# Kernel tuning notes

Measured on AMD Instinct MI355X. Metric: run time of the kernel, lower is better.

Reference implementation:

```python
import jax, jax.numpy as jnp
import numpy as np
from math import sqrt

B, T, C = 2, 2048, 2048
H = 16
NOPE, ROPE, VD, LORA = 128, 64, 128, 512
QK = NOPE + ROPE  # 192
EPS = 1e-6


def _make_freq_cis(T, rope_dim):
    inv = 1.0 / (10000.0 ** (np.arange(0, rope_dim, 2, dtype=np.float32) / rope_dim))
    t = np.arange(T, dtype=np.float32)
    ang = np.outer(t, inv)  # [T, rope_dim/2]
    return jnp.asarray(np.stack([np.cos(ang), np.sin(ang)], -1))  # [T, rope_dim/2, 2]


def setup_inputs() -> dict:
    key = jax.random.key(0)
    ks = jax.random.split(key, 6)
    x = jax.random.normal(ks[0], (B, T, C), jnp.float32)
    freq_cis = _make_freq_cis(T, ROPE)
    causal = jnp.where(jnp.tril(jnp.ones((T, T), bool)), 0.0, -1e9).astype(jnp.float32)
    Wq = jax.random.normal(ks[1], (C, H * QK), jnp.float32) * (1.0 / sqrt(C))
    Wckv = jax.random.normal(ks[2], (C, LORA + ROPE), jnp.float32) * (1.0 / sqrt(C))
    kv_norm_w = jnp.ones((LORA,), jnp.float32)
    Wdkv = jax.random.normal(ks[3], (LORA, H * (NOPE + VD)), jnp.float32) * (1.0 / sqrt(LORA))
    Wproj = jax.random.normal(ks[4], (H * VD, C), jnp.float32) * (1.0 / sqrt(H * VD))
    return {"x": x, "freq_cis": freq_cis, "mask": causal, "window": causal,
            "Wq": Wq, "Wckv": Wckv, "kv_norm_w": kv_norm_w, "Wdkv": Wdkv,
            "Wproj": Wproj, "start_pos": 0}


def apply_rope(x, freq_cis):
    # x: [B, T, h, D]; freq_cis: [T, D/2, 2]
    b, t, h, d = x.shape
    xr = x.reshape(b, t, h, d // 2, 2)
    fc = freq_cis.reshape(1, t, 1, d // 2, 2)
    real = xr[..., 0] * fc[..., 0] - xr[..., 1] * fc[..., 1]
    imag = xr[..., 1] * fc[..., 0] + xr[..., 0] * fc[..., 1]
    return jnp.stack([real, imag], -1).reshape(b, t, h, d)


def rms_norm(x, w, eps=EPS):
    return x * jax.lax.rsqrt(jnp.mean(x * x, -1, keepdims=True) + eps) * w


def reference(x, freq_cis, mask, window, Wq, Wckv, kv_norm_w, Wdkv, Wproj, start_pos):
    del window, start_pos  # Global attention, no KV cache (prefill)
    b, t, _ = x.shape
    q = (x @ Wq).reshape(b, t, H, QK)
    q_nope, q_rope = q[..., :NOPE], q[..., NOPE:]
    q_rope = apply_rope(q_rope, freq_cis)

    ckv = x @ Wckv  # [B, T, LORA+ROPE]
    kv_lat, k_rope = ckv[..., :LORA], ckv[..., LORA:]
    k_rope = apply_rope(k_rope.reshape(b, t, 1, ROPE), freq_cis)  # [B,T,1,ROPE]

    kv = rms_norm(kv_lat, kv_norm_w) @ Wdkv  # [B, T, H*(NOPE+VD)]
    kv = kv.reshape(b, t, H, NOPE + VD)
    k_nope, v = kv[..., :NOPE], kv[..., NOPE:]

    q = jnp.concatenate([q_nope, q_rope], -1)                                   # [B,T,H,QK]
    k = jnp.concatenate([k_nope, jnp.broadcast_to(k_rope, (b, t, H, ROPE))], -1)

    scale = 1.0 / sqrt(QK)
    atten = jnp.einsum('bqhd,bkhd->bhqk', q, k) * scale + mask  # [B,H,T,T]
    atten = jax.nn.softmax(atten, -1)
    out = jnp.einsum('bhqk,bkhd->bqhd', atten, v).reshape(b, t, H * VD)
    return out @ Wproj
```

## Files before the change

### kernel.cpp

```cpp
#include <hip/hip_runtime.h>
#include <hip/hip_bf16.h>
#include <math.h>


typedef short bf16x8 __attribute__((ext_vector_type(8)));
typedef float f32x4 __attribute__((ext_vector_type(4)));

#define MFMA16(a, b, c) __builtin_amdgcn_mfma_f32_16x16x32_bf16(a, b, c, 0, 0, 0)

__device__ __forceinline__ short f2bf(float f) {
  union { float f; unsigned u; } v; v.f = f;
  unsigned r = v.u + 0x7fffu + ((v.u >> 16) & 1u);
  return (short)(r >> 16);
}
__device__ __forceinline__ float bf2f(short s) {
  union { unsigned u; float f; } v;
  v.u = ((unsigned)(unsigned short)s) << 16;
  return v.f;
}
__device__ __forceinline__ void gl16(const void* g, void* l) {
  __builtin_amdgcn_global_load_lds(
      (const __attribute__((address_space(1))) unsigned int*)g,
      (__attribute__((address_space(3))) unsigned int*)l, 16, 0, 0);
}
#define CFENCE() asm volatile("" ::: "memory")
#define HWBAR()  do { CFENCE(); __builtin_amdgcn_s_barrier(); CFENCE(); } while (0)

__global__ __launch_bounds__(256) void cvt_k(const float* __restrict__ in,
                                             short* __restrict__ out, int n) {
  int i = (blockIdx.x * 256 + threadIdx.x) * 8;
  if (i >= n) return;
  float4 a = *(const float4*)(in + i);
  float4 b = *(const float4*)(in + i + 4);
  bf16x8 o;
  o[0] = f2bf(a.x); o[1] = f2bf(a.y); o[2] = f2bf(a.z); o[3] = f2bf(a.w);
  o[4] = f2bf(b.x); o[5] = f2bf(b.y); o[6] = f2bf(b.z); o[7] = f2bf(b.w);
  *(bf16x8*)(out + i) = o;
}

__global__ __launch_bounds__(256) void tcvt_k(const float* __restrict__ W,
                                              short* __restrict__ out,
                                              int K, int N, int Np, int row_off) {
  __shared__ float tile[32][33];
  int k0 = blockIdx.x * 32, n0 = blockIdx.y * 32;
  int tx = threadIdx.x & 31, ty = threadIdx.x >> 5;
#pragma unroll
  for (int j = 0; j < 4; j++) {
    int k = k0 + ty + j * 8, n = n0 + tx;
    tile[ty + j * 8][tx] = (n < N) ? W[(size_t)k * N + n] : 0.f;
  }
  __syncthreads();
#pragma unroll
  for (int j = 0; j < 4; j++) {
    int n = n0 + ty + j * 8;
    out[(size_t)(row_off + n) * K + k0 + tx] = f2bf(tile[tx][ty + j * 8]);
  }
}

template <int MODE, int BM, int BN, int SGL>
__global__ __launch_bounds__(512, 2) void gemm8_k(const short* __restrict__ A,
                                                  const short* __restrict__ Bt,
                                                  void* __restrict__ C1,
                                                  void* __restrict__ C2,
                                                  int M, int N, int K, int nbx) {
  constexpr int FM = BM / 32;
  constexpr int FN = BN / 64;
  constexpr int XCH = (BM * 4) / 512;
  constexpr int YCH = (BN * 4) / 512;
  __shared__ short lX[3][BM * 32];
  __shared__ short lY[3][BN * 32];

  const int nwg = gridDim.x;
  const int cpx = nwg >> 3;
  const int swz = (blockIdx.x & 7) * cpx + (blockIdx.x >> 3);
  const int bx = swz % nbx, by = swz / nbx;
  const int m0 = bx * BM, n0 = by * BN;
  const int tid = threadIdx.x, lane = tid & 63, wave = tid >> 6;
  const int wm = wave >> 2, wn = wave & 3;
  const int l15 = lane & 15, l4 = lane >> 4;
  const int nt = K >> 5;

  auto stage = [&](int t) {
    int kk = t << 5;
    short* bX = &lX[t % 3][0];
    short* bY = &lY[t % 3][0];
#pragma unroll
    for (int c = 0; c < XCH; c++) {
      int idx = c * 512 + tid;
      int row = idx >> 2, seg = idx & 3;
      gl16(A + (size_t)(m0 + row) * K + kk + ((seg ^ ((row >> 1) & 3)) << 3),
           bX + idx * 8);
    }
#pragma unroll
    for (int c = 0; c < YCH; c++) {
      int idx = c * 512 + tid;
      int row = idx >> 2, seg = idx & 3;
      gl16(Bt + (size_t)(n0 + row) * K + kk + ((seg ^ ((row >> 1) & 3)) << 3),
           bY + idx * 8);
    }
  };

  f32x4 zero = {0.f, 0.f, 0.f, 0.f};
  f32x4 acc[FM][FN];
#pragma unroll
  for (int i = 0; i < FM; i++)
#pragma unroll
    for (int j = 0; j < FN; j++) acc[i][j] = zero;

  stage(0);
  stage(1);
  if constexpr (SGL == 4) asm volatile("s_waitcnt vmcnt(4)" ::: "memory");
  else                    asm volatile("s_waitcnt vmcnt(3)" ::: "memory");
  HWBAR();

  for (int t = 0; t < nt; t++) {
    const short* bX = &lX[t % 3][0];
    const short* bY = &lY[t % 3][0];
    bf16x8 xf[FM / 2], yf[FN];
#pragma unroll
    for (int i = 0; i < FM / 2; i++) {
      int row = wm * (BM / 2) + i * 16 + l15;
      xf[i] = *(const bf16x8*)&bX[row * 32 + ((l4 ^ ((row >> 1) & 3)) << 3)];
    }
#pragma unroll
    for (int j = 0; j < FN; j++) {
      int row = wn * (BN / 4) + j * 16 + l15;
      yf[j] = *(const bf16x8*)&bY[row * 32 + ((l4 ^ ((row >> 1) & 3)) << 3)];
    }
    bool st = (t + 2 < nt);
    if (st) stage(t + 2);
    HWBAR();
    __builtin_amdgcn_sched_barrier(0);
    __builtin_amdgcn_s_setprio(1);
#pragma unroll
    for (int i = 0; i < FM / 2; i++)
#pragma unroll
      for (int j = 0; j < FN; j++) acc[i][j] = MFMA16(xf[i], yf[j], acc[i][j]);
    __builtin_amdgcn_s_setprio(0);
    bf16x8 xg[FM / 2];
#pragma unroll
    for (int i = 0; i < FM / 2; i++) {
      int row = wm * (BM / 2) + (FM / 2 + i) * 16 + l15;
      xg[i] = *(const bf16x8*)&bX[row * 32 + ((l4 ^ ((row >> 1) & 3)) << 3)];
    }
    if (st) {
      if constexpr (SGL == 4) asm volatile("s_waitcnt vmcnt(4) lgkmcnt(0)" ::: "memory");
      else                    asm volatile("s_waitcnt vmcnt(3) lgkmcnt(0)" ::: "memory");
    } else {
      asm volatile("s_waitcnt vmcnt(0) lgkmcnt(0)" ::: "memory");
    }
    HWBAR();
    __builtin_amdgcn_sched_barrier(0);
    __builtin_amdgcn_s_setprio(1);
#pragma unroll
    for (int i = 0; i < FM / 2; i++)
#pragma unroll
      for (int j = 0; j < FN; j++)
        acc[FM / 2 + i][j] = MFMA16(xg[i], yf[j], acc[FM / 2 + i][j]);
    __builtin_amdgcn_s_setprio(0);
  }

#pragma unroll
  for (int i = 0; i < FM; i++) {
#pragma unroll
    for (int j = 0; j < FN; j++) {
#pragma unroll
      for (int r = 0; r < 4; r++) {
        int m = m0 + wm * (BM / 2) + i * 16 + l4 * 4 + r;
        int n = n0 + wn * (BN / 4) + j * 16 + l15;
        if (n >= N) continue;
        float v = acc[i][j][r];
        if (MODE == 0) {
          ((short*)C1)[(size_t)m * N + n] = f2bf(v);
        } else if (MODE == 1) {
          ((float*)C1)[(size_t)m * N + n] = v;
        } else {
          int bb = m >> 11, t2 = m & 2047, hh = n >> 8, c = n & 255;
          if (c < 128)
            ((short*)C1)[((size_t)(bb * 16 + hh) * 2048 + t2) * 192 + c] = f2bf(v);
          else
            ((short*)C2)[((size_t)(bb * 16 + hh) * 128 + (c - 128)) * 2048 + t2] = f2bf(v);
        }
      }
    }
  }
}

__global__ __launch_bounds__(256) void rmsnorm_k(const short* __restrict__ qc,
                                                 const float* __restrict__ w,
                                                 short* __restrict__ out) {
  int row = blockIdx.x * 4 + (threadIdx.x >> 6);
  int lane = threadIdx.x & 63;
  const short* src = qc + (size_t)row * 3712 + 3072 + lane * 8;
  bf16x8 v = *(const bf16x8*)src;
  float f[8];
  float ss = 0.f;
#pragma unroll
  for (int j = 0; j < 8; j++) { f[j] = bf2f(v[j]); ss += f[j] * f[j]; }
#pragma unroll
  for (int m = 1; m < 64; m <<= 1) ss += __shfl_xor(ss, m);
  float r = rsqrtf(ss * (1.f / 512.f) + 1e-6f);
  bf16x8 o;
#pragma unroll
  for (int j = 0; j < 8; j++) o[j] = f2bf(f[j] * r * w[lane * 8 + j]);
  *(bf16x8*)(out + (size_t)row * 512 + lane * 8) = o;
}

__global__ __launch_bounds__(256) void qrope_k(const short* __restrict__ qc,
                                               const float* __restrict__ freq,
                                               short* __restrict__ q_all) {
  int row = blockIdx.x * 4 + (threadIdx.x >> 6);
  int lane = threadIdx.x & 63;
  int b = row >> 15, h = (row >> 11) & 15, t = row & 2047;
  const short* src = qc + (size_t)(b * 2048 + t) * 3712 + h * 192;
  short* dst = q_all + (size_t)row * 192;
  const float scale = 0.07216878364870323f;
  dst[lane] = f2bf(bf2f(src[lane]) * scale);
  dst[lane + 64] = f2bf(bf2f(src[lane + 64]) * scale);
  int p = lane >> 1;
  float c = freq[t * 64 + p * 2], s = freq[t * 64 + p * 2 + 1];
  float x0 = bf2f(src[128 + 2 * p]), x1 = bf2f(src[128 + 2 * p + 1]);
  float v = (lane & 1) ? (x1 * c + x0 * s) : (x0 * c - x1 * s);
  dst[128 + lane] = f2bf(v * scale);
}

__global__ __launch_bounds__(64) void krope_k(const short* __restrict__ qc,
                                              const float* __restrict__ freq,
                                              short* __restrict__ k_all) {
  int bt = blockIdx.x;
  int lane = threadIdx.x;
  int b = bt >> 11, t = bt & 2047;
  const short* src = qc + (size_t)bt * 3712 + 3584;
  int p = lane >> 1;
  float c = freq[t * 64 + p * 2], s = freq[t * 64 + p * 2 + 1];
  float x0 = bf2f(src[2 * p]), x1 = bf2f(src[2 * p + 1]);
  float v = (lane & 1) ? (x1 * c + x0 * s) : (x0 * c - x1 * s);
  short vb = f2bf(v);
#pragma unroll
  for (int h = 0; h < 16; h++)
    k_all[((size_t)(b * 16 + h) * 2048 + t) * 192 + 128 + lane] = vb;
}

__device__ __forceinline__ void stage_kv8(const short* __restrict__ Kp,
                                          const short* __restrict__ VT,
                                          short* kb, short* vb, int kt, int tid) {
#pragma unroll
  for (int i = 0; i < 3; i++) {
    int idx = i * 512 + tid;
    if (idx < 768) {
      int row = idx / 24, seg = idx % 24;
      gl16(Kp + (size_t)(kt + row) * 192 + (seg ^ (row & 7)) * 8, kb + idx * 8);
    } else if (idx < 1280) {
      int v = idx - 768;
      int row = v >> 2, seg = v & 3;
      gl16(VT + (size_t)row * 2048 + kt + (seg ^ ((row >> 1) & 3)) * 8, vb + v * 8);
    }
  }
}

__global__ __launch_bounds__(512) void attn_k(const short* __restrict__ q_all,
                                              const short* __restrict__ k_all,
                                              const short* __restrict__ vt,
                                              short* __restrict__ attn_out) {
  __shared__ short kbuf[2][32 * 192];
  __shared__ short vbuf[2][128 * 32];
  __shared__ short pbuf[8][16 * 40];
  int bh = blockIdx.x;
  int b = bh >> 4, h = bh & 15;
  int col = gridDim.y - 1 - blockIdx.y;
  int tid = threadIdx.x;
  int wave = tid >> 6, lane = tid & 63;
  int l15 = lane & 15, l4 = lane >> 4;
  int qbase = col * 128 + wave * 16;
  const short* Q = q_all + ((size_t)bh * 2048 + qbase) * 192;
  const short* Kp = k_all + (size_t)bh * 2048 * 192;
  const short* VT = vt + (size_t)bh * 128 * 2048;

  bf16x8 qf[6];
#pragma unroll
  for (int k0 = 0; k0 < 6; k0++)
    qf[k0] = *(const bf16x8*)(Q + l15 * 192 + k0 * 32 + l4 * 8);

  f32x4 zero = {0.f, 0.f, 0.f, 0.f};
  f32x4 o[8];
#pragma unroll
  for (int n = 0; n < 8; n++) o[n] = zero;
  float lsum[4] = {0.f, 0.f, 0.f, 0.f};

  const int kend = col * 128 + 128;
  const int qmax = qbase + 15;

  stage_kv8(Kp, VT, kbuf[0], vbuf[0], 0, tid);
  __syncthreads();

  for (int kt = 0; kt < kend; kt += 32) {
    int cur = (kt >> 5) & 1;
    if (kt + 32 < kend)
      stage_kv8(Kp, VT, kbuf[cur ^ 1], vbuf[cur ^ 1], kt + 32, tid);

    if (kt <= qmax) {
      f32x4 s0 = zero, s1 = zero;
#pragma unroll
      for (int k0 = 0; k0 < 6; k0++) {
        int r0 = l15, r1 = 16 + l15;
        bf16x8 kf0 = *(const bf16x8*)&kbuf[cur][r0 * 192 + (((k0 << 2) + l4) ^ (r0 & 7)) * 8];
        bf16x8 kf1 = *(const bf16x8*)&kbuf[cur][r1 * 192 + (((k0 << 2) + l4) ^ (r1 & 7)) * 8];
        s0 = MFMA16(qf[k0], kf0, s0);
        s1 = MFMA16(qf[k0], kf1, s1);
      }
#pragma unroll
      for (int r = 0; r < 4; r++) {
        int qi = qbase + l4 * 4 + r;
        float p0 = (kt + l15 <= qi) ? __expf(s0[r] - 20.f) : 0.f;
        float p1 = (kt + 16 + l15 <= qi) ? __expf(s1[r] - 20.f) : 0.f;
        lsum[r] += p0 + p1;
        pbuf[wave][(l4 * 4 + r) * 40 + l15] = f2bf(p0);
        pbuf[wave][(l4 * 4 + r) * 40 + 16 + l15] = f2bf(p1);
      }
      asm volatile("s_waitcnt lgkmcnt(0)" ::: "memory");
      __builtin_amdgcn_sched_barrier(0);
      bf16x8 pf = *(const bf16x8*)&pbuf[wave][l15 * 40 + l4 * 8];
#pragma unroll
      for (int n = 0; n < 8; n++) {
        int row = n * 16 + l15;
        bf16x8 vf = *(const bf16x8*)&vbuf[cur][row * 32 + ((l4 ^ ((row >> 1) & 3))) * 8];
        o[n] = MFMA16(pf, vf, o[n]);
      }
    }
    __syncthreads();
  }

#pragma unroll
  for (int r = 0; r < 4; r++) {
    float s = lsum[r];
    s += __shfl_xor(s, 1);
    s += __shfl_xor(s, 2);
    s += __shfl_xor(s, 4);
    s += __shfl_xor(s, 8);
    float inv = 1.f / s;
    int qi = qbase + l4 * 4 + r;
    size_t base = ((size_t)b * 2048 + qi) * 2048 + h * 128;
#pragma unroll
    for (int n = 0; n < 8; n++)
      attn_out[base + n * 16 + l15] = f2bf(o[n][r] * inv);
  }
}

extern "C" void kernel_launch(void* const* d_in, const int* in_sizes, int n_in,
                              void* d_out, int out_size, void* d_ws, size_t ws_size,
                              hipStream_t stream) {
  const float* x = (const float*)d_in[0];
  const float* freq = (const float*)d_in[1];
  const float* Wq = (const float*)d_in[4];
  const float* Wckv = (const float*)d_in[5];
  const float* kvw = (const float*)d_in[6];
  const float* Wdkv = (const float*)d_in[7];
  const float* Wproj = (const float*)d_in[8];

  char* ws = (char*)d_ws;
  size_t off = 0;
  auto alloc = [&](size_t bytes) {
    size_t o = off;
    off += (bytes + 255) & ~(size_t)255;
    return o;
  };
  size_t o_xbf = alloc(4096ull * 2048 * 2);
  size_t o_wqc = alloc(3840ull * 2048 * 2);
  size_t o_wdkv = alloc(4096ull * 512 * 2);
  size_t o_wproj = alloc(2048ull * 2048 * 2);
  size_t o_qc = alloc(4096ull * 3712 * 2);
  size_t o_kvlat = alloc(4096ull * 512 * 2);
  size_t o_qall = alloc(32ull * 2048 * 192 * 2);
  size_t o_kall = alloc(32ull * 2048 * 192 * 2);
  size_t o_vt = alloc(32ull * 128 * 2048 * 2);
  size_t o_attn = o_xbf;

  short* x_bf = (short*)(ws + o_xbf);
  short* wqc = (short*)(ws + o_wqc);
  short* wdkv = (short*)(ws + o_wdkv);
  short* wproj = (short*)(ws + o_wproj);
  short* qc = (short*)(ws + o_qc);
  short* kvlat = (short*)(ws + o_kvlat);
  short* qall = (short*)(ws + o_qall);
  short* kall = (short*)(ws + o_kall);
  short* vtb = (short*)(ws + o_vt);
  short* attnb = (short*)(ws + o_attn);

  cvt_k<<<4096, 256, 0, stream>>>(x, x_bf, 4096 * 2048);
  tcvt_k<<<dim3(64, 96), 256, 0, stream>>>(Wq, wqc, 2048, 3072, 3072, 0);
  tcvt_k<<<dim3(64, 24), 256, 0, stream>>>(Wckv, wqc, 2048, 576, 768, 3072);
  tcvt_k<<<dim3(16, 128), 256, 0, stream>>>(Wdkv, wdkv, 512, 4096, 4096, 0);
  tcvt_k<<<dim3(64, 64), 256, 0, stream>>>(Wproj, wproj, 2048, 2048, 2048, 0);

  gemm8_k<0, 256, 256, 4><<<240, 512, 0, stream>>>(x_bf, wqc, qc, nullptr,
                                                   4096, 3712, 2048, 16);

  rmsnorm_k<<<1024, 256, 0, stream>>>(qc, kvw, kvlat);
  qrope_k<<<16384, 256, 0, stream>>>(qc, freq, qall);
  krope_k<<<4096, 64, 0, stream>>>(qc, freq, kall);

  gemm8_k<2, 256, 256, 4><<<256, 512, 0, stream>>>(kvlat, wdkv, kall, vtb,
                                                   4096, 4096, 512, 16);

  attn_k<<<dim3(32, 16), 512, 0, stream>>>(qall, kall, vtb, attnb);

  gemm8_k<1, 128, 256, 3><<<256, 512, 0, stream>>>(attnb, wproj, d_out, nullptr,
                                                   4096, 2048, 2048, 32);
}
```

Measured before the change: 288.1 us.

## Rewrite attention kernel with 32x32 MFMA and register-resident probabilities

The attention kernel moves from 16x16x32 MFMA tiles with 8 waves to 32x32x16 MFMA tiles with 4 waves, each wave covering 32 queries. Scores are computed transposed (K as A operand), so the probability tile already sits in the layout the PV MFMA wants. That removes the LDS round-trip through pbuf and its wait. The scale now folds in log2(e) so exp2f can be used, and fully unmasked tiles skip the causal comparisons. Probabilities are packed with v_cvt_pk_bf16_f32, and the output is written as packed pairs. Risks are the complex lane-to-row swizzle mapping and fewer waves per block, which could lower latency hiding.

```diff
diff --git a/kernel.cpp b/kernel.cpp
--- a/kernel.cpp
+++ b/kernel.cpp
@@ -5,8 +5,10 @@
 
 typedef short bf16x8 __attribute__((ext_vector_type(8)));
 typedef float f32x4 __attribute__((ext_vector_type(4)));
+typedef float f32x16 __attribute__((ext_vector_type(16)));
 
 #define MFMA16(a, b, c) __builtin_amdgcn_mfma_f32_16x16x32_bf16(a, b, c, 0, 0, 0)
+#define MFMA32(a, b, c) __builtin_amdgcn_mfma_f32_32x32x16_bf16(a, b, c, 0, 0, 0)
 
 __device__ __forceinline__ short f2bf(float f) {
   union { float f; unsigned u; } v; v.f = f;
@@ -17,6 +19,11 @@
   union { unsigned u; float f; } v;
   v.u = ((unsigned)(unsigned short)s) << 16;
   return v.f;
+}
+__device__ __forceinline__ unsigned cvtpk(float a, float b) {
+  unsigned r;
+  asm("v_cvt_pk_bf16_f32 %0, %1, %2" : "=v"(r) : "v"(a), "v"(b));
+  return r;
 }
 __device__ __forceinline__ void gl16(const void* g, void* l) {
   __builtin_amdgcn_global_load_lds(
@@ -214,7 +221,7 @@
   int b = row >> 15, h = (row >> 11) & 15, t = row & 2047;
   const short* src = qc + (size_t)(b * 2048 + t) * 3712 + h * 192;
   short* dst = q_all + (size_t)row * 192;
-  const float scale = 0.07216878364870323f;
+  const float scale = 0.10411756f;
   dst[lane] = f2bf(bf2f(src[lane]) * scale);
   dst[lane + 64] = f2bf(bf2f(src[lane + 64]) * scale);
   int p = lane >> 1;
@@ -241,108 +248,127 @@
     k_all[((size_t)(b * 16 + h) * 2048 + t) * 192 + 128 + lane] = vb;
 }
 
-__device__ __forceinline__ void stage_kv8(const short* __restrict__ Kp,
+__device__ __forceinline__ void stage_kv4(const short* __restrict__ Kp,
                                           const short* __restrict__ VT,
                                           short* kb, short* vb, int kt, int tid) {
 #pragma unroll
   for (int i = 0; i < 3; i++) {
-    int idx = i * 512 + tid;
-    if (idx < 768) {
-      int row = idx / 24, seg = idx % 24;
-      gl16(Kp + (size_t)(kt + row) * 192 + (seg ^ (row & 7)) * 8, kb + idx * 8);
-    } else if (idx < 1280) {
-      int v = idx - 768;
-      int row = v >> 2, seg = v & 3;
-      gl16(VT + (size_t)row * 2048 + kt + (seg ^ ((row >> 1) & 3)) * 8, vb + v * 8);
-    }
-  }
-}
-
-__global__ __launch_bounds__(512) void attn_k(const short* __restrict__ q_all,
+    int idx = i * 256 + tid;
+    int row = idx / 24, seg = idx % 24;
+    gl16(Kp + (size_t)(kt + row) * 192 + ((seg ^ (row & 7)) << 3), kb + idx * 8);
+  }
+#pragma unroll
+  for (int i = 0; i < 2; i++) {
+    int v = i * 256 + tid;
+    int row = v >> 2, seg = v & 3;
+    gl16(VT + (size_t)row * 2048 + kt + ((seg ^ ((row >> 1) & 3)) << 3), vb + v * 8);
+  }
+}
+
+__global__ __launch_bounds__(256) void attn_k(const short* __restrict__ q_all,
                                               const short* __restrict__ k_all,
                                               const short* __restrict__ vt,
                                               short* __restrict__ attn_out) {
   __shared__ short kbuf[2][32 * 192];
   __shared__ short vbuf[2][128 * 32];
-  __shared__ short pbuf[8][16 * 40];
   int bh = blockIdx.x;
   int b = bh >> 4, h = bh & 15;
   int col = gridDim.y - 1 - blockIdx.y;
   int tid = threadIdx.x;
   int wave = tid >> 6, lane = tid & 63;
-  int l15 = lane & 15, l4 = lane >> 4;
-  int qbase = col * 128 + wave * 16;
-  const short* Q = q_all + ((size_t)bh * 2048 + qbase) * 192;
+  int l31 = lane & 31, hi = lane >> 5;
+  int qw = col * 128 + wave * 32;
+  int qrow = qw + l31;
+  const short* Q = q_all + ((size_t)bh * 2048 + qrow) * 192;
   const short* Kp = k_all + (size_t)bh * 2048 * 192;
   const short* VT = vt + (size_t)bh * 128 * 2048;
-
-  bf16x8 qf[6];
-#pragma unroll
-  for (int k0 = 0; k0 < 6; k0++)
-    qf[k0] = *(const bf16x8*)(Q + l15 * 192 + k0 * 32 + l4 * 8);
-
-  f32x4 zero = {0.f, 0.f, 0.f, 0.f};
-  f32x4 o[8];
-#pragma unroll
-  for (int n = 0; n < 8; n++) o[n] = zero;
-  float lsum[4] = {0.f, 0.f, 0.f, 0.f};
+  int sig = (l31 & 19) | ((l31 >> 1) & 4) | ((l31 << 1) & 8);
+  int s7 = sig & 7;
+
+  bf16x8 qf[12];
+#pragma unroll
+  for (int kb = 0; kb < 12; kb++)
+    qf[kb] = *(const bf16x8*)(Q + kb * 16 + hi * 8);
+
+  f32x16 o[4];
+#pragma unroll
+  for (int vb = 0; vb < 4; vb++)
+#pragma unroll
+    for (int r = 0; r < 16; r++) o[vb][r] = 0.f;
+  f32x16 sInit;
+#pragma unroll
+  for (int r = 0; r < 16; r++) sInit[r] = -28.8539f;
+  float lsum = 0.f;
 
   const int kend = col * 128 + 128;
-  const int qmax = qbase + 15;
-
-  stage_kv8(Kp, VT, kbuf[0], vbuf[0], 0, tid);
+
+  stage_kv4(Kp, VT, kbuf[0], vbuf[0], 0, tid);
   __syncthreads();
 
   for (int kt = 0; kt < kend; kt += 32) {
     int cur = (kt >> 5) & 1;
     if (kt + 32 < kend)
-      stage_kv8(Kp, VT, kbuf[cur ^ 1], vbuf[cur ^ 1], kt + 32, tid);
-
-    if (kt <= qmax) {
-      f32x4 s0 = zero, s1 = zero;
-#pragma unroll
-      for (int k0 = 0; k0 < 6; k0++) {
-        int r0 = l15, r1 = 16 + l15;
-        bf16x8 kf0 = *(const bf16x8*)&kbuf[cur][r0 * 192 + (((k0 << 2) + l4) ^ (r0 & 7)) * 8];
-        bf16x8 kf1 = *(const bf16x8*)&kbuf[cur][r1 * 192 + (((k0 << 2) + l4) ^ (r1 & 7)) * 8];
-        s0 = MFMA16(qf[k0], kf0, s0);
-        s1 = MFMA16(qf[k0], kf1, s1);
+      stage_kv4(Kp, VT, kbuf[cur ^ 1], vbuf[cur ^ 1], kt + 32, tid);
+
+    if (kt < qw + 32) {
+      f32x16 sc = sInit;
+#pragma unroll
+      for (int kb = 0; kb < 12; kb++) {
+        int c = 2 * kb + hi;
+        bf16x8 kf = *(const bf16x8*)&kbuf[cur][sig * 192 + ((c ^ s7) << 3)];
+        sc = MFMA32(kf, qf[kb], sc);
       }
-#pragma unroll
-      for (int r = 0; r < 4; r++) {
-        int qi = qbase + l4 * 4 + r;
-        float p0 = (kt + l15 <= qi) ? __expf(s0[r] - 20.f) : 0.f;
-        float p1 = (kt + 16 + l15 <= qi) ? __expf(s1[r] - 20.f) : 0.f;
-        lsum[r] += p0 + p1;
-        pbuf[wave][(l4 * 4 + r) * 40 + l15] = f2bf(p0);
-        pbuf[wave][(l4 * 4 + r) * 40 + 16 + l15] = f2bf(p1);
+      unsigned pw[8];
+      if (kt + 32 <= qw) {
+#pragma unroll
+        for (int r2 = 0; r2 < 8; r2++) {
+          float pa = exp2f(sc[2 * r2]);
+          float pb = exp2f(sc[2 * r2 + 1]);
+          lsum += pa + pb;
+          pw[r2] = cvtpk(pa, pb);
+        }
+      } else {
+#pragma unroll
+        for (int r2 = 0; r2 < 8; r2++) {
+          int r = 2 * r2;
+          int key = kt + (r & 3) + 4 * ((r >> 2) & 1) + 8 * hi + 16 * (r >> 3);
+          float va = (key <= qrow) ? sc[r] : -1e30f;
+          float vb2 = (key + 1 <= qrow) ? sc[r + 1] : -1e30f;
+          float pa = exp2f(va);
+          float pb = exp2f(vb2);
+          lsum += pa + pb;
+          pw[r2] = cvtpk(pa, pb);
+        }
       }
-      asm volatile("s_waitcnt lgkmcnt(0)" ::: "memory");
-      __builtin_amdgcn_sched_barrier(0);
-      bf16x8 pf = *(const bf16x8*)&pbuf[wave][l15 * 40 + l4 * 8];
-#pragma unroll
-      for (int n = 0; n < 8; n++) {
-        int row = n * 16 + l15;
-        bf16x8 vf = *(const bf16x8*)&vbuf[cur][row * 32 + ((l4 ^ ((row >> 1) & 3))) * 8];
-        o[n] = MFMA16(pf, vf, o[n]);
+      union { unsigned u[4]; bf16x8 v; } p0, p1;
+#pragma unroll
+      for (int w = 0; w < 4; w++) { p0.u[w] = pw[w]; p1.u[w] = pw[4 + w]; }
+#pragma unroll
+      for (int vb = 0; vb < 4; vb++) {
+        int vcol = vb * 32 + l31;
+        int sw = (vcol >> 1) & 3;
+        bf16x8 vf0 = *(const bf16x8*)&vbuf[cur][vcol * 32 + ((hi ^ sw) << 3)];
+        bf16x8 vf1 = *(const bf16x8*)&vbuf[cur][vcol * 32 + (((2 + hi) ^ sw) << 3)];
+        o[vb] = MFMA32(vf0, p0.v, o[vb]);
+        o[vb] = MFMA32(vf1, p1.v, o[vb]);
       }
     }
     __syncthreads();
   }
 
-#pragma unroll
-  for (int r = 0; r < 4; r++) {
-    float s = lsum[r];
-    s += __shfl_xor(s, 1);
-    s += __shfl_xor(s, 2);
-    s += __shfl_xor(s, 4);
-    s += __shfl_xor(s, 8);
-    float inv = 1.f / s;
-    int qi = qbase + l4 * 4 + r;
-    size_t base = ((size_t)b * 2048 + qi) * 2048 + h * 128;
-#pragma unroll
-    for (int n = 0; n < 8; n++)
-      attn_out[base + n * 16 + l15] = f2bf(o[n][r] * inv);
+  lsum += __shfl_xor(lsum, 32);
+  float inv = 1.f / lsum;
+  size_t base = ((size_t)b * 2048 + qrow) * 2048 + h * 128;
+#pragma unroll
+  for (int vb = 0; vb < 4; vb++) {
+#pragma unroll
+    for (int r2 = 0; r2 < 8; r2++) {
+      int r = 2 * r2;
+      int v = vb * 32 + (r & 3) + 8 * (r >> 2) + 4 * hi;
+      unsigned pk2 = ((unsigned)(unsigned short)f2bf(o[vb][r] * inv)) |
+                     (((unsigned)(unsigned short)f2bf(o[vb][r + 1] * inv)) << 16);
+      *(unsigned*)(attn_out + base + v) = pk2;
+    }
   }
 }
 
@@ -402,7 +428,7 @@
   gemm8_k<2, 256, 256, 4><<<256, 512, 0, stream>>>(kvlat, wdkv, kall, vtb,
                                                    4096, 4096, 512, 16);
 
-  attn_k<<<dim3(32, 16), 512, 0, stream>>>(qall, kall, vtb, attnb);
+  attn_k<<<dim3(32, 16), 256, 0, stream>>>(qall, kall, vtb, attnb);
 
   gemm8_k<1, 128, 256, 3><<<256, 512, 0, stream>>>(attnb, wproj, d_out, nullptr,
                                                    4096, 2048, 2048, 32);
```

Measured after the change: 314.4 us. 9.2% more time.
